# Kernel optimization log

Measured on AMD Instinct MI355X. Metric: run time of the kernel, lower is better.

## Reference

```python
import jax, jax.numpy as jnp
import numpy as np

B, S, D = 128, 144, 1024  # batch, grid tokens (12x12), d_model
GRID = 12


def _relative_position(grid_size):
    # Reconstructs get_grids_pos for a grid_size x grid_size grid of unit cells
    # (x_min = cell col/row index, x_max = x_min + 1), standard grid-feature layout.
    x = jnp.arange(grid_size, dtype=jnp.float32)
    px_min = jnp.repeat(x, grid_size)          # (S,) varies slowly (rows)
    py_min = jnp.tile(x, grid_size)            # (S,) varies fast (cols)
    px_max = px_min + 1.0
    py_max = py_min + 1.0
    cx = (px_min + px_max) * 0.5
    cy = (py_min + py_max) * 0.5
    w = px_max - px_min + 1.0                  # == 2 everywhere
    h = py_max - py_min + 1.0
    eps = 1e-10
    dx = jnp.log(jnp.maximum(jnp.abs((cx[:, None] - cx[None, :]) / w[:, None]), eps))
    dy = jnp.log(jnp.maximum(jnp.abs((cy[:, None] - cy[None, :]) / h[:, None]), eps))
    dw = jnp.log(w[:, None] / w[None, :])
    dh = jnp.log(h[:, None] / h[None, :])
    return jnp.stack([dx, dy, dw, dh], axis=-1)  # (S, S, 4)


def setup_inputs() -> dict:
    key = jax.random.key(0)
    ks = jax.random.split(key, 12)
    std = 0.02
    return {
        "query": jax.random.normal(ks[0], (B, S, D), jnp.float32),
        "key":   jax.random.normal(ks[1], (B, S, D), jnp.float32),
        "value": jax.random.normal(ks[2], (B, S, D), jnp.float32),
        # Linear weights stored as (in, out): y = x @ W + b
        "Wq": jax.random.normal(ks[3], (D, D), jnp.float32) * std,
        "bq": jnp.zeros((D,), jnp.float32),
        "Wk": jax.random.normal(ks[4], (D, D), jnp.float32) * std,
        "bk": jnp.zeros((D,), jnp.float32),
        "Wv": jax.random.normal(ks[5], (D, D), jnp.float32) * std,
        "bv": jnp.zeros((D,), jnp.float32),
        "Wl": jax.random.normal(ks[6], (4, D), jnp.float32) * std,
        "bl": jnp.zeros((D,), jnp.float32),
        "w_g": jax.random.normal(ks[7], (S, D, 1), jnp.float32) * std,
    }


def reference(query, key, value, Wq, bq, Wk, bk, Wv, bv, Wl, bl, w_g):
    d_model = query.shape[-1]
    scale = d_model ** (-0.5)
    act = jax.nn.relu  # get_activation_function() assumed relu; dropout=0 (eval)

    q = act(query @ Wq + bq)   # (B,S,D)
    k = act(key @ Wk + bk)
    v = act(value @ Wv + bv)

    attn = jnp.einsum('bid,bjd->bij', q, k) * scale  # (B,S,S)

    seq = value.shape[1]
    pos = _relative_position(int(round(seq ** 0.5)))  # (S,S,4)
    rel = act(pos @ Wl + bl)                          # (S,S,D)
    # torch.matmul(rela_pos, w_g): row i of the grid uses w_g[i]
    bias = act(jnp.einsum('ijd,id->ij', rel, w_g[..., 0]))  # (S,S)

    attn = jax.nn.softmax(attn + bias[None, :, :], axis=-1)
    return jnp.einsum('bij,bjd->bid', attn, v)
```

## Files before the change

### kernel.cpp

```cpp
#include <hip/hip_runtime.h>
#include <hip/hip_bf16.h>
#include <stdint.h>

#define SS 144
#define DD 1024
#define NB 128
#define SP 160
#define SCALE 0.03125f

typedef __attribute__((ext_vector_type(8))) short short8;
typedef __attribute__((ext_vector_type(4))) float floatx4;
typedef unsigned short u16;

#define MFMA(a, b, c) __builtin_amdgcn_mfma_f32_16x16x32_bf16((a), (b), (c), 0, 0, 0)

__device__ __forceinline__ u16 f2bf(float f) {
    union { float f; unsigned int i; } v; v.f = f;
    unsigned int r = v.i + 0x7fff + ((v.i >> 16) & 1);
    return (u16)(r >> 16);
}
__device__ __forceinline__ short8 pack8(float4 a, float4 b) {
    short8 r;
    r[0] = (short)f2bf(a.x); r[1] = (short)f2bf(a.y);
    r[2] = (short)f2bf(a.z); r[3] = (short)f2bf(a.w);
    r[4] = (short)f2bf(b.x); r[5] = (short)f2bf(b.y);
    r[6] = (short)f2bf(b.z); r[7] = (short)f2bf(b.w);
    return r;
}

__device__ __forceinline__ void gload16(u16* lds, const u16* g) {
    __builtin_amdgcn_global_load_lds(
        (__attribute__((address_space(1))) void*)g,
        (__attribute__((address_space(3))) void*)lds, 16, 0, 0);
}

__global__ __launch_bounds__(256) void convert3_k(
    const float* __restrict__ Xq, const float* __restrict__ Xk,
    const float* __restrict__ Xv,
    u16* __restrict__ Oq, u16* __restrict__ Ok, u16* __restrict__ Ov, int nchunk) {
    int z = blockIdx.y;
    const float* X = z == 0 ? Xq : (z == 1 ? Xk : Xv);
    u16* O = z == 0 ? Oq : (z == 1 ? Ok : Ov);
    for (int c = blockIdx.x * 256 + threadIdx.x; c < nchunk; c += gridDim.x * 256) {
        size_t i = (size_t)c * 8;
        float4 a = *(const float4*)(X + i);
        float4 b = *(const float4*)(X + i + 4);
        *(short8*)(O + i) = pack8(a, b);
    }
}

__global__ void transpose_w_k(const float* __restrict__ Wq, const float* __restrict__ Wk,
                              const float* __restrict__ Wv, u16* __restrict__ WT) {
    __shared__ u16 t[32][33];
    int z = blockIdx.z;
    const float* W = z == 0 ? Wq : (z == 1 ? Wk : Wv);
    u16* O = WT + (size_t)z * DD * DD;
    int bn = blockIdx.x * 32, bk = blockIdx.y * 32;
    int tx = threadIdx.x & 31, ty = threadIdx.x >> 5;
    for (int r = ty; r < 32; r += 8) t[r][tx] = f2bf(W[(size_t)(bk + r) * DD + bn + tx]);
    __syncthreads();
    for (int r = ty; r < 32; r += 8) O[(size_t)(bn + r) * DD + bk + tx] = t[tx][r];
}

__global__ void bias_k(const float* __restrict__ Wl, const float* __restrict__ bl,
                       const float* __restrict__ wg, float* __restrict__ biasb) {
    int ij = blockIdx.x;
    int i = ij / SS, j = ij - i * SS;
    int lane = threadIdx.x;
    int ri = i / 12, ci = i - ri * 12, rj = j / 12, cj = j - rj * 12;
    float dx = logf(fmaxf(fabsf((float)(ri - rj)) * 0.5f, 1e-10f));
    float dy = logf(fmaxf(fabsf((float)(ci - cj)) * 0.5f, 1e-10f));
    float s = 0.f;
    for (int d = lane; d < DD; d += 64) {
        float r = dx * Wl[d] + dy * Wl[DD + d] + bl[d];
        r = fmaxf(r, 0.f);
        s += r * wg[(size_t)i * DD + d];
    }
    #pragma unroll
    for (int m = 32; m > 0; m >>= 1) s += __shfl_xor(s, m);
    if (lane == 0) biasb[ij] = fmaxf(s, 0.f);
}

__global__ __launch_bounds__(256) void proj_k(
    const u16* __restrict__ Xq, const u16* __restrict__ Xk, const u16* __restrict__ Xv,
    const u16* __restrict__ WT,
    const float* __restrict__ bq, const float* __restrict__ bk, const float* __restrict__ bv,
    u16* __restrict__ Oq, u16* __restrict__ Ok, u16* __restrict__ OvT) {
    __shared__ __align__(16) u16 As[128 * 32];
    __shared__ __align__(16) u16 Bs[128 * 32];
    int z = blockIdx.z;
    const u16* Xb = z == 0 ? Xq : (z == 1 ? Xk : Xv);
    const u16* Wt = WT + (size_t)z * DD * DD;
    const float* bias = z == 0 ? bq : (z == 1 ? bk : bv);
    int bn = blockIdx.x, bm = blockIdx.y;
    int tid = threadIdx.x, lane = tid & 63, wv = tid >> 6;
    int wm = wv >> 1, wn = wv & 1;
    int lr = lane & 15, lq = lane >> 4;

    floatx4 zero4 = {0.f, 0.f, 0.f, 0.f};
    floatx4 acc[4][4];
    #pragma unroll
    for (int r = 0; r < 4; r++)
        #pragma unroll
        for (int c = 0; c < 4; c++) acc[r][c] = zero4;

    const u16* Abase = Xb + (size_t)bm * 128 * DD;
    const u16* Bbase = Wt + (size_t)bn * 128 * DD;

    int c0 = tid, c1 = tid + 256;
    const u16* ga0 = Abase + (size_t)(c0 >> 2) * DD + ((c0 & 3) << 3);
    const u16* ga1 = Abase + (size_t)(c1 >> 2) * DD + ((c1 & 3) << 3);
    const u16* gb0 = Bbase + (size_t)(c0 >> 2) * DD + ((c0 & 3) << 3);
    const u16* gb1 = Bbase + (size_t)(c1 >> 2) * DD + ((c1 & 3) << 3);
    u16* la0 = &As[c0 * 8];
    u16* la1 = &As[c1 * 8];
    u16* lb0 = &Bs[c0 * 8];
    u16* lb1 = &Bs[c1 * 8];

    for (int k0 = 0; k0 < DD; k0 += 32) {
        __syncthreads();
        gload16(la0, ga0 + k0);
        gload16(la1, ga1 + k0);
        gload16(lb0, gb0 + k0);
        gload16(lb1, gb1 + k0);
        __syncthreads();
        short8 a[4], b[4];
        #pragma unroll
        for (int r = 0; r < 4; r++)
            a[r] = *(const short8*)&As[(wm * 64 + r * 16 + lr) * 32 + lq * 8];
        #pragma unroll
        for (int c = 0; c < 4; c++)
            b[c] = *(const short8*)&Bs[(wn * 64 + c * 16 + lr) * 32 + lq * 8];
        #pragma unroll
        for (int r = 0; r < 4; r++)
            #pragma unroll
            for (int c = 0; c < 4; c++)
                acc[r][c] = MFMA(a[r], b[c], acc[r][c]);
    }

    int mrow0 = bm * 128 + wm * 64;
    int ncol0 = bn * 128 + wn * 64;
    if (z < 2) {
        u16* O = z == 0 ? Oq : Ok;
        #pragma unroll
        for (int r = 0; r < 4; r++)
            #pragma unroll
            for (int c = 0; c < 4; c++) {
                int col = ncol0 + c * 16 + lr;
                float bb = bias[col];
                #pragma unroll
                for (int i = 0; i < 4; i++) {
                    int row = mrow0 + r * 16 + lq * 4 + i;
                    O[(size_t)row * DD + col] = f2bf(fmaxf(acc[r][c][i] + bb, 0.f));
                }
            }
    } else {
        #pragma unroll
        for (int r = 0; r < 4; r++)
            #pragma unroll
            for (int c = 0; c < 4; c++) {
                int col = ncol0 + c * 16 + lr;
                float bb = bias[col];
                #pragma unroll
                for (int i = 0; i < 4; i++) {
                    int row = mrow0 + r * 16 + lq * 4 + i;
                    int bidx = row / SS;
                    int srow = row - bidx * SS;
                    OvT[((size_t)bidx * DD + col) * SP + srow] =
                        f2bf(fmaxf(acc[r][c][i] + bb, 0.f));
                }
            }
    }
}

__global__ __launch_bounds__(256) void attn_k(
    const u16* __restrict__ q, const u16* __restrict__ k,
    const float* __restrict__ biasb, u16* __restrict__ probs) {
    __shared__ float Sst[16][148];
    int it = blockIdx.x, b = blockIdx.y;
    int i0 = it * 16;
    int tid = threadIdx.x, lane = tid & 63, wv = tid >> 6;
    int lr = lane & 15, lq = lane >> 4;
    const u16* qs = q + ((size_t)b * SS + i0) * DD;
    const u16* ks = k + (size_t)b * SS * DD;

    floatx4 zero4 = {0.f, 0.f, 0.f, 0.f};
    floatx4 acc[3] = {zero4, zero4, zero4};
    int nt = (wv == 0) ? 3 : 2;

    for (int d0 = 0; d0 < DD; d0 += 32) {
        short8 a = *(const short8*)&qs[(size_t)lr * DD + d0 + lq * 8];
        #pragma unroll
        for (int m = 0; m < 3; m++) {
            if (m < nt) {
                int t = wv + m * 4;
                short8 bb = *(const short8*)&ks[(size_t)(t * 16 + lr) * DD + d0 + lq * 8];
                acc[m] = MFMA(a, bb, acc[m]);
            }
        }
    }
    for (int m = 0; m < nt; m++) {
        int t = wv + m * 4;
        #pragma unroll
        for (int i = 0; i < 4; i++) {
            int row = lq * 4 + i, col = t * 16 + lr;
            Sst[row][col] = acc[m][i] * SCALE + biasb[(i0 + row) * SS + col];
        }
    }
    __syncthreads();

    int g = tid >> 4, j = tid & 15;
    float mx = -1e30f;
    for (int c = j; c < SS; c += 16) mx = fmaxf(mx, Sst[g][c]);
    #pragma unroll
    for (int m = 1; m < 16; m <<= 1) mx = fmaxf(mx, __shfl_xor(mx, m));
    float sm = 0.f;
    float ev[9];
    int t = 0;
    for (int c = j; c < SS; c += 16, t++) { float e = expf(Sst[g][c] - mx); ev[t] = e; sm += e; }
    #pragma unroll
    for (int m = 1; m < 16; m <<= 1) sm += __shfl_xor(sm, m);
    float inv = 1.f / sm;
    u16* pr = probs + ((size_t)b * SS + i0 + g) * SP;
    t = 0;
    for (int c = j; c < SP; c += 16, t++) {
        float val = (c < SS) ? ev[t < 9 ? t : 8] * inv : 0.f;
        pr[c] = f2bf(val);
    }
}

__global__ __launch_bounds__(256) void pv_k(
    const u16* __restrict__ probs, const u16* __restrict__ vT, float* __restrict__ out) {
    int cb = blockIdx.x, it = blockIdx.y, b = blockIdx.z;
    int tid = threadIdx.x, lane = tid & 63, wv = tid >> 6;
    int lr = lane & 15, lq = lane >> 4;
    const u16* pr = probs + ((size_t)b * SS + it * 16) * SP;
    const u16* vt = vT + (size_t)b * DD * SP;
    int col0 = cb * 256 + wv * 64;

    floatx4 zero4 = {0.f, 0.f, 0.f, 0.f};
    floatx4 acc[4] = {zero4, zero4, zero4, zero4};
    for (int k0 = 0; k0 < SP; k0 += 32) {
        short8 a = *(const short8*)&pr[(size_t)lr * SP + k0 + lq * 8];
        #pragma unroll
        for (int c = 0; c < 4; c++) {
            short8 bb = *(const short8*)&vt[(size_t)(col0 + c * 16 + lr) * SP + k0 + lq * 8];
            acc[c] = MFMA(a, bb, acc[c]);
        }
    }
    #pragma unroll
    for (int c = 0; c < 4; c++)
        #pragma unroll
        for (int i = 0; i < 4; i++) {
            int row = it * 16 + lq * 4 + i, col = col0 + c * 16 + lr;
            out[((size_t)b * SS + row) * DD + col] = acc[c][i];
        }
}

extern "C" void kernel_launch(void* const* d_in, const int* in_sizes, int n_in,
                              void* d_out, int out_size, void* d_ws, size_t ws_size,
                              hipStream_t stream) {
    const float* query = (const float*)d_in[0];
    const float* key_  = (const float*)d_in[1];
    const float* value = (const float*)d_in[2];
    const float* Wq = (const float*)d_in[3];
    const float* bq = (const float*)d_in[4];
    const float* Wk = (const float*)d_in[5];
    const float* bk = (const float*)d_in[6];
    const float* Wv = (const float*)d_in[7];
    const float* bv = (const float*)d_in[8];
    const float* Wl = (const float*)d_in[9];
    const float* bl = (const float*)d_in[10];
    const float* wg = (const float*)d_in[11];

    u16* WT    = (u16*)d_ws;
    u16* Xv    = WT + (size_t)3 * DD * DD;
    u16* q     = Xv + (size_t)NB * SS * DD;
    u16* k     = q  + (size_t)NB * SS * DD;
    u16* vT    = k  + (size_t)NB * SS * DD;
    u16* probs = vT + (size_t)NB * DD * SP;
    float* biasb = (float*)(probs + (size_t)NB * SS * SP);

    u16* Xq = (u16*)d_out;
    u16* Xk = Xq + (size_t)NB * SS * DD;

    transpose_w_k<<<dim3(32, 32, 3), 256, 0, stream>>>(Wq, Wk, Wv, WT);
    bias_k<<<dim3(SS * SS), 64, 0, stream>>>(Wl, bl, wg, biasb);

    int nchunk = NB * SS * DD / 8;
    convert3_k<<<dim3(1024, 3), 256, 0, stream>>>(query, key_, value, Xq, Xk, Xv, nchunk);
    proj_k<<<dim3(8, 144, 3), 256, 0, stream>>>(Xq, Xk, Xv, WT, bq, bk, bv, q, k, vT);

    attn_k<<<dim3(9, NB), 256, 0, stream>>>(q, k, biasb, probs);
    pv_k<<<dim3(4, 9, NB), 256, 0, stream>>>(probs, vT, (float*)d_out);
}
```

Measured before the change: 622.1 us.

## Fuse softmax and PV into attention kernel; swap projection grid order

Merges the attention-score/softmax kernel with the probs×V kernel: probabilities are now held in shared memory as bf16 and each block computes the full 1024-wide output for its 16 rows, removing the global probs buffer and one launch. The projection grid is also reordered so consecutive blocks walk M tiles under the same weight column tile, which changes L2 reuse. The cost is that the fused kernel has only 9x128 blocks, each doing a 16-iteration serial PV loop with 4 waves, so parallelism per block drops compared with the separate pv kernel's larger grid.

```diff
diff --git a/kernel.cpp b/kernel.cpp
--- a/kernel.cpp
+++ b/kernel.cpp
@@ -92,7 +92,7 @@
     const u16* Xb = z == 0 ? Xq : (z == 1 ? Xk : Xv);
     const u16* Wt = WT + (size_t)z * DD * DD;
     const float* bias = z == 0 ? bq : (z == 1 ? bk : bv);
-    int bn = blockIdx.x, bm = blockIdx.y;
+    int bm = blockIdx.x, bn = blockIdx.y;
     int tid = threadIdx.x, lane = tid & 63, wv = tid >> 6;
     int wm = wv >> 1, wn = wv & 1;
     int lr = lane & 15, lq = lane >> 4;
@@ -173,10 +173,12 @@
     }
 }
 
-__global__ __launch_bounds__(256) void attn_k(
+__global__ __launch_bounds__(256) void attn_pv_k(
     const u16* __restrict__ q, const u16* __restrict__ k,
-    const float* __restrict__ biasb, u16* __restrict__ probs) {
+    const u16* __restrict__ vT, const float* __restrict__ biasb,
+    float* __restrict__ out) {
     __shared__ float Sst[16][148];
+    __shared__ __align__(16) u16 Pst[16][168];
     int it = blockIdx.x, b = blockIdx.y;
     int i0 = it * 16;
     int tid = threadIdx.x, lane = tid & 63, wv = tid >> 6;
@@ -209,52 +211,43 @@
     }
     __syncthreads();
 
-    int g = tid >> 4, j = tid & 15;
-    float mx = -1e30f;
-    for (int c = j; c < SS; c += 16) mx = fmaxf(mx, Sst[g][c]);
-    #pragma unroll
-    for (int m = 1; m < 16; m <<= 1) mx = fmaxf(mx, __shfl_xor(mx, m));
-    float sm = 0.f;
-    float ev[9];
-    int t = 0;
-    for (int c = j; c < SS; c += 16, t++) { float e = expf(Sst[g][c] - mx); ev[t] = e; sm += e; }
-    #pragma unroll
-    for (int m = 1; m < 16; m <<= 1) sm += __shfl_xor(sm, m);
-    float inv = 1.f / sm;
-    u16* pr = probs + ((size_t)b * SS + i0 + g) * SP;
-    t = 0;
-    for (int c = j; c < SP; c += 16, t++) {
-        float val = (c < SS) ? ev[t < 9 ? t : 8] * inv : 0.f;
-        pr[c] = f2bf(val);
-    }
-}
-
-__global__ __launch_bounds__(256) void pv_k(
-    const u16* __restrict__ probs, const u16* __restrict__ vT, float* __restrict__ out) {
-    int cb = blockIdx.x, it = blockIdx.y, b = blockIdx.z;
-    int tid = threadIdx.x, lane = tid & 63, wv = tid >> 6;
-    int lr = lane & 15, lq = lane >> 4;
-    const u16* pr = probs + ((size_t)b * SS + it * 16) * SP;
+    {
+        int g = tid >> 4, j = tid & 15;
+        float mx = -1e30f;
+        for (int c = j; c < SS; c += 16) mx = fmaxf(mx, Sst[g][c]);
+        #pragma unroll
+        for (int m = 1; m < 16; m <<= 1) mx = fmaxf(mx, __shfl_xor(mx, m));
+        float sm = 0.f;
+        float ev[9];
+        int t = 0;
+        for (int c = j; c < SS; c += 16, t++) { float e = expf(Sst[g][c] - mx); ev[t] = e; sm += e; }
+        #pragma unroll
+        for (int m = 1; m < 16; m <<= 1) sm += __shfl_xor(sm, m);
+        float inv = 1.f / sm;
+        t = 0;
+        for (int c = j; c < SP; c += 16, t++) {
+            float val = (c < SS) ? ev[t < 9 ? t : 8] * inv : 0.f;
+            Pst[g][c] = f2bf(val);
+        }
+    }
+    __syncthreads();
+
     const u16* vt = vT + (size_t)b * DD * SP;
-    int col0 = cb * 256 + wv * 64;
-
-    floatx4 zero4 = {0.f, 0.f, 0.f, 0.f};
-    floatx4 acc[4] = {zero4, zero4, zero4, zero4};
-    for (int k0 = 0; k0 < SP; k0 += 32) {
-        short8 a = *(const short8*)&pr[(size_t)lr * SP + k0 + lq * 8];
-        #pragma unroll
-        for (int c = 0; c < 4; c++) {
-            short8 bb = *(const short8*)&vt[(size_t)(col0 + c * 16 + lr) * SP + k0 + lq * 8];
-            acc[c] = MFMA(a, bb, acc[c]);
-        }
-    }
-    #pragma unroll
-    for (int c = 0; c < 4; c++)
-        #pragma unroll
-        for (int i = 0; i < 4; i++) {
-            int row = it * 16 + lq * 4 + i, col = col0 + c * 16 + lr;
-            out[((size_t)b * SS + row) * DD + col] = acc[c][i];
-        }
+    float* ob = out + ((size_t)b * SS + i0) * DD;
+    #pragma unroll 4
+    for (int m = 0; m < 16; m++) {
+        int colb = wv * 256 + m * 16;
+        floatx4 pacc = zero4;
+        #pragma unroll
+        for (int k0 = 0; k0 < SP; k0 += 32) {
+            short8 a = *(const short8*)&Pst[lr][k0 + lq * 8];
+            short8 bb = *(const short8*)&vt[(size_t)(colb + lr) * SP + k0 + lq * 8];
+            pacc = MFMA(a, bb, pacc);
+        }
+        #pragma unroll
+        for (int i = 0; i < 4; i++)
+            ob[(size_t)(lq * 4 + i) * DD + colb + lr] = pacc[i];
+    }
 }
 
 extern "C" void kernel_launch(void* const* d_in, const int* in_sizes, int n_in,
@@ -278,8 +271,7 @@
     u16* q     = Xv + (size_t)NB * SS * DD;
     u16* k     = q  + (size_t)NB * SS * DD;
     u16* vT    = k  + (size_t)NB * SS * DD;
-    u16* probs = vT + (size_t)NB * DD * SP;
-    float* biasb = (float*)(probs + (size_t)NB * SS * SP);
+    float* biasb = (float*)(vT + (size_t)NB * DD * SP);
 
     u16* Xq = (u16*)d_out;
     u16* Xk = Xq + (size_t)NB * SS * DD;
@@ -289,8 +281,7 @@
 
     int nchunk = NB * SS * DD / 8;
     convert3_k<<<dim3(1024, 3), 256, 0, stream>>>(query, key_, value, Xq, Xk, Xv, nchunk);
-    proj_k<<<dim3(8, 144, 3), 256, 0, stream>>>(Xq, Xk, Xv, WT, bq, bk, bv, q, k, vT);
-
-    attn_k<<<dim3(9, NB), 256, 0, stream>>>(q, k, biasb, probs);
-    pv_k<<<dim3(4, 9, NB), 256, 0, stream>>>(probs, vT, (float*)d_out);
-}
+    proj_k<<<dim3(144, 8, 3), 256, 0, stream>>>(Xq, Xk, Xv, WT, bq, bk, bv, q, k, vT);
+
+    attn_pv_k<<<dim3(9, NB), 256, 0, stream>>>(q, k, vT, biasb, (float*)d_out);
+}
```

New measurement: 644.6 us. 1.04x slower.
